# Performance work log

Measured on AMD Instinct MI355X. Metric: run time of the kernel, lower is better.

## Reference

```python
import jax, jax.numpy as jnp
import numpy as np

N_NODES = 100000
N_EDGES = 1600000
IN_CH = 128
NHIDDEN = 64
OUT_CH = 40
NLAYERS = 4
ALPHA = 0.1


def setup_inputs() -> dict:
    key = jax.random.key(0)
    ks = jax.random.split(key, 7)
    x = jax.random.normal(ks[0], (N_NODES, IN_CH), dtype=jnp.float32)
    edge_index = jax.random.randint(ks[1], (2, N_EDGES), 0, N_NODES, dtype=jnp.int64)
    batch_graph = jnp.zeros((N_NODES,), dtype=jnp.int64)
    fc1_w = jax.random.normal(ks[2], (NHIDDEN, IN_CH), dtype=jnp.float32) * (1.0 / np.sqrt(IN_CH))
    fc1_b = jax.random.normal(ks[3], (NHIDDEN,), dtype=jnp.float32) * 0.01
    conv_w = jax.random.normal(ks[4], (NLAYERS, NHIDDEN, NHIDDEN), dtype=jnp.float32) * (1.0 / np.sqrt(NHIDDEN))
    fc2_w = jax.random.normal(ks[5], (OUT_CH, NHIDDEN), dtype=jnp.float32) * (1.0 / np.sqrt(NHIDDEN))
    fc2_b = jax.random.normal(ks[6], (OUT_CH,), dtype=jnp.float32) * 0.01
    return {"x": x, "edge_index": edge_index, "batch_graph": batch_graph,
            "fc1_w": fc1_w, "fc1_b": fc1_b, "conv_w": conv_w,
            "fc2_w": fc2_w, "fc2_b": fc2_b}


def reference(x, edge_index, batch_graph, fc1_w, fc1_b, conv_w, fc2_w, fc2_b):
    # eval mode: dropout layers are identity
    n = x.shape[0]
    row, col = edge_index[0], edge_index[1]  # source, target

    # gcn_norm with add_self_loops=False: sym deg^-1/2 normalization
    deg = jax.ops.segment_sum(jnp.ones_like(row, dtype=x.dtype), col, num_segments=n)
    dinv = jnp.where(deg > 0, deg ** -0.5, 0.0)
    norm = (dinv[row] * dinv[col])[:, None]  # [E, 1]

    h = jax.nn.relu(x @ fc1_w.T + fc1_b)  # [N, nhidden]
    h0 = h
    nlayers = conv_w.shape[0]
    for i in range(nlayers):
        # GCN2Conv: aggregate, initial-residual mix, weight1 matmul (beta=1)
        agg = jax.ops.segment_sum(h[row] * norm, col, num_segments=n)
        mixed = (1.0 - ALPHA) * agg + ALPHA * h0
        h = jax.nn.relu(mixed @ conv_w[i])
    out = h @ fc2_w.T + fc2_b  # [N, out_channels]
    return out
```

## Files before the change

### kernel.cpp

```cpp
#include <hip/hip_runtime.h>
#include <hip/hip_fp16.h>

#define N_NODES 100000
#define N_EDGES 1600000
#define IN_CH   128
#define NHID    64
#define OUT_CH  40
#define NBLK    391
#define NBUCK   196
#define BCAP    8960
#define ECAP    1024


__global__ __launch_bounds__(256) void k_scan1(const int* __restrict__ cnt,
                                               int* __restrict__ rowptr,
                                               int* __restrict__ bsum) {
    __shared__ int s[256];
    int t = threadIdx.x;
    int n = blockIdx.x * 256 + t;
    int v = (n < N_NODES) ? cnt[n] : 0;
    s[t] = v;
    __syncthreads();
    for (int off = 1; off < 256; off <<= 1) {
        int add = (t >= off) ? s[t - off] : 0;
        __syncthreads();
        s[t] += add;
        __syncthreads();
    }
    int incl = s[t];
    if (n < N_NODES) rowptr[n] = incl - v;
    if (t == 255) bsum[blockIdx.x] = incl;
}

__global__ __launch_bounds__(512) void k_scan2(int* __restrict__ bsum) {
    __shared__ int s[512];
    int t = threadIdx.x;
    int v = (t < NBLK) ? bsum[t] : 0;
    s[t] = v;
    __syncthreads();
    for (int off = 1; off < 512; off <<= 1) {
        int add = (t >= off) ? s[t - off] : 0;
        __syncthreads();
        s[t] += add;
        __syncthreads();
    }
    if (t < NBLK) bsum[t] = s[t] - v;
}

__global__ __launch_bounds__(256) void k_scan3(const int* __restrict__ cnt,
                                               const int* __restrict__ bsum,
                                               int* __restrict__ rowptr,
                                               float* __restrict__ dinv) {
    int n = blockIdx.x * 256 + threadIdx.x;
    if (n < N_NODES) {
        int rp = rowptr[n] + bsum[n >> 8];
        rowptr[n] = rp;
        int c = cnt[n];
        dinv[n] = (c > 0) ? rsqrtf((float)c) : 0.0f;
    }
    if (blockIdx.x == 0 && threadIdx.x == 0) rowptr[N_NODES] = N_EDGES;
}


__global__ __launch_bounds__(256) void k_scatA(const int* __restrict__ ei,
                                               int* __restrict__ bucketCnt,
                                               int2* __restrict__ ebufA) {
    __shared__ int hist[NBUCK];
    __shared__ int base[NBUCK];
    int t = threadIdx.x;
    int chunk = blockIdx.x * 4096;
    for (int i = t; i < NBUCK; i += 256) hist[i] = 0;
    __syncthreads();
#pragma unroll 4
    for (int i = 0; i < 16; i++) {
        int e = chunk + i * 256 + t;
        if (e < N_EDGES) atomicAdd(&hist[ei[N_EDGES + e] >> 9], 1);
    }
    __syncthreads();
    for (int b = t; b < NBUCK; b += 256) {
        int h = hist[b];
        base[b] = h ? atomicAdd(&bucketCnt[b], h) : 0;
    }
    __syncthreads();
#pragma unroll 4
    for (int i = 0; i < 16; i++) {
        int e = chunk + i * 256 + t;
        if (e < N_EDGES) {
            int r = ei[e], c = ei[N_EDGES + e];
            int pos = atomicAdd(&base[c >> 9], 1);
            ebufA[(size_t)(c >> 9) * BCAP + pos] = make_int2(r, c);
        }
    }
}


__global__ __launch_bounds__(256) void k_deg(const int2* __restrict__ ebufA,
                                             const int* __restrict__ bucketCnt,
                                             int* __restrict__ cnt) {
    __shared__ int hist[512];
    int b = blockIdx.x;
    int nodeB = b * 512;
    int t = threadIdx.x;
    for (int i = t; i < 512; i += 256) hist[i] = 0;
    __syncthreads();
    int nE = bucketCnt[b];
    const int2* src = ebufA + (size_t)b * BCAP;
    for (int i = t; i < nE; i += 256) atomicAdd(&hist[src[i].y - nodeB], 1);
    __syncthreads();
    for (int i = t; i < 512; i += 256) {
        int node = nodeB + i;
        if (node < N_NODES) cnt[node] = hist[i];
    }
}


__global__ __launch_bounds__(256) void k_scatB(const int2* __restrict__ ebufA,
                                               const int* __restrict__ bucketCnt,
                                               const int* __restrict__ rowptr,
                                               int* __restrict__ e4) {
    __shared__ int lcur[512];
    int b = blockIdx.x;
    int nodeB = b * 512;
    int t = threadIdx.x;
    for (int i = t; i < 512; i += 256) {
        int node = nodeB + i;
        lcur[i] = (node < N_NODES) ? rowptr[node] : 0;
    }
    __syncthreads();
    int nE = bucketCnt[b];
    const int2* src = ebufA + (size_t)b * BCAP;
    for (int i = t; i < nE; i += 256) {
        int2 rc = src[i];
        int pos = atomicAdd(&lcur[rc.y - nodeB], 1);
        e4[pos] = rc.x;
    }
}

__device__ __forceinline__ void store_h4(__half* dst, float a, float b, float c, float d) {
    union { uint2 u; __half2 h[2]; } pk;
    pk.h[0] = __floats2half2_rn(a, b);
    pk.h[1] = __floats2half2_rn(c, d);
    *(uint2*)dst = pk.u;
}


__global__ __launch_bounds__(256, 4) void k_fc1(const float* __restrict__ x,
                                                const float* __restrict__ w,
                                                const float* __restrict__ b,
                                                const float* __restrict__ dinv,
                                                __half* __restrict__ h016,
                                                __half* __restrict__ hs1) {
    __shared__ float xs[64 * 128];
    int t = threadIdx.x;
    int nodeBase = blockIdx.x * 64;

    {
        int lane8 = t & 7, rhalf = t >> 3;
#pragma unroll
        for (int r2 = 0; r2 < 2; r2++) {
            int nl = r2 * 32 + rhalf;
            int n = nodeBase + nl;
            int swz = (nl ^ (nl >> 3)) & 7;
            float4* dstrow = (float4*)(xs + nl * 128);
            if (n < N_NODES) {
                const float4* src = (const float4*)(x + (size_t)n * IN_CH);
#pragma unroll
                for (int q = 0; q < 4; q++) dstrow[(q * 8 + lane8) ^ swz] = src[q * 8 + lane8];
            } else {
                float4 z = {0.f, 0.f, 0.f, 0.f};
#pragma unroll
                for (int q = 0; q < 4; q++) dstrow[(q * 8 + lane8) ^ swz] = z;
            }
        }
    }
    __syncthreads();

    int tx = t & 15, ty = t >> 4;
    int n0 = tx * 4, o0 = ty * 4;
    int swz0 = ((n0 + 0) ^ ((n0 + 0) >> 3)) & 7;
    int swz1 = ((n0 + 1) ^ ((n0 + 1) >> 3)) & 7;
    int swz2 = ((n0 + 2) ^ ((n0 + 2) >> 3)) & 7;
    int swz3 = ((n0 + 3) ^ ((n0 + 3) >> 3)) & 7;
    const float4* xrow0 = (const float4*)(xs + (n0 + 0) * 128);
    const float4* xrow1 = (const float4*)(xs + (n0 + 1) * 128);
    const float4* xrow2 = (const float4*)(xs + (n0 + 2) * 128);
    const float4* xrow3 = (const float4*)(xs + (n0 + 3) * 128);

    float c[4][4];
#pragma unroll
    for (int i = 0; i < 4; i++)
#pragma unroll
        for (int j = 0; j < 4; j++) c[i][j] = 0.f;

#pragma unroll 4
    for (int k = 0; k < IN_CH; k += 4) {
        int kk = k >> 2;
        float4 b0 = *(const float4*)&w[(size_t)(o0 + 0) * IN_CH + k];
        float4 b1 = *(const float4*)&w[(size_t)(o0 + 1) * IN_CH + k];
        float4 b2 = *(const float4*)&w[(size_t)(o0 + 2) * IN_CH + k];
        float4 b3 = *(const float4*)&w[(size_t)(o0 + 3) * IN_CH + k];
        float4 a0 = xrow0[kk ^ swz0];
        float4 a1 = xrow1[kk ^ swz1];
        float4 a2 = xrow2[kk ^ swz2];
        float4 a3 = xrow3[kk ^ swz3];
#pragma unroll
        for (int i = 0; i < 4; i++) {
            float4 a = (i == 0) ? a0 : (i == 1) ? a1 : (i == 2) ? a2 : a3;
            c[i][0] = fmaf(a.x, b0.x, fmaf(a.y, b0.y, fmaf(a.z, b0.z, fmaf(a.w, b0.w, c[i][0]))));
            c[i][1] = fmaf(a.x, b1.x, fmaf(a.y, b1.y, fmaf(a.z, b1.z, fmaf(a.w, b1.w, c[i][1]))));
            c[i][2] = fmaf(a.x, b2.x, fmaf(a.y, b2.y, fmaf(a.z, b2.z, fmaf(a.w, b2.w, c[i][2]))));
            c[i][3] = fmaf(a.x, b3.x, fmaf(a.y, b3.y, fmaf(a.z, b3.z, fmaf(a.w, b3.w, c[i][3]))));
        }
    }

    float4 bias = *(const float4*)&b[o0];
#pragma unroll
    for (int i = 0; i < 4; i++) {
        int n = nodeBase + n0 + i;
        if (n < N_NODES) {
            float vx = fmaxf(c[i][0] + bias.x, 0.f);
            float vy = fmaxf(c[i][1] + bias.y, 0.f);
            float vz = fmaxf(c[i][2] + bias.z, 0.f);
            float vw = fmaxf(c[i][3] + bias.w, 0.f);
            store_h4(&h016[(size_t)n * NHID + o0], vx, vy, vz, vw);
            float dn = dinv[n];
            store_h4(&hs1[(size_t)n * NHID + o0], vx * dn, vy * dn, vz * dn, vw * dn);
        }
    }
}


__global__ __launch_bounds__(256, 4) void k_conv(const __half* __restrict__ hs,
                                                 const __half* __restrict__ h0,
                                                 const int* __restrict__ rowptr,
                                                 const int* __restrict__ e4,
                                                 const float* __restrict__ W,
                                                 const float* __restrict__ dinv,
                                                 __half* __restrict__ hout,
                                                 int scaled) {
    __shared__ int   eS[ECAP];
    __shared__ float mix[32 * 68];
    int t = threadIdx.x;
    int nodeBase = blockIdx.x * 32;
    int grp = t >> 3;
    int cg = (t & 7) * 8;

    int n = nodeBase + grp;
    int s = rowptr[n], e = rowptr[n + 1];
    int base0 = rowptr[nodeBase];
    int nE = rowptr[nodeBase + 32] - base0;
    int nStage = (nE < ECAP) ? nE : ECAP;
    for (int i = t; i < nStage; i += 256) eS[i] = e4[base0 + i];

#define LOADM_G(pm, jb)                                                  \
    {                                                                    \
        _Pragma("unroll")                                                \
        for (int u = 0; u < 4; u++) {                                    \
            int idx = (jb) + u;                                          \
            pm[u] = (idx < e) ? e4[idx] : N_NODES;                       \
        }                                                                \
    }
#define LOADM(pm, jb)                                                    \
    {                                                                    \
        _Pragma("unroll")                                                \
        for (int u = 0; u < 4; u++) {                                    \
            int idx = (jb) + u;                                          \
            int m = N_NODES;                                             \
            if (idx < e) {                                               \
                int li = idx - base0;                                    \
                m = (li < ECAP) ? eS[li] : e4[idx];                      \
            }                                                            \
            pm[u] = m;                                                   \
        }                                                                \
    }
#define ISSUE(pv, pm)                                                    \
    {                                                                    \
        _Pragma("unroll")                                                \
        for (int u = 0; u < 4; u++)                                      \
            pv[u] = *(const float4*)&hs[(size_t)pm[u] * NHID + cg];      \
    }
#define ACC4(cv)                                                         \
    {                                                                    \
        _Pragma("unroll")                                                \
        for (int u = 0; u < 4; u++) {                                    \
            const __half2* hp = (const __half2*)&cv[u];                  \
            _Pragma("unroll")                                            \
            for (int q = 0; q < 4; q++) {                                \
                float2 f = __half22float2(hp[q]);                        \
                acc[q * 2 + 0] += f.x;                                   \
                acc[q * 2 + 1] += f.y;                                   \
            }                                                            \
        }                                                                \
    }

    int    pmA[4], pmB[4];
    float4 pvA[4], pvB[4];
    LOADM_G(pmA, s);     ISSUE(pvA, pmA);
    LOADM_G(pmB, s + 4); ISSUE(pvB, pmB);

    float dn = dinv[n];
    float4 h0raw = *(const float4*)&h0[(size_t)n * NHID + cg];

    float acc[8];
#pragma unroll
    for (int i = 0; i < 8; i++) acc[i] = 0.f;

    __syncthreads();

    for (int j = s; j < e; j += 8) {
        {
            float4 cv[4];
#pragma unroll
            for (int u = 0; u < 4; u++) cv[u] = pvA[u];
            int jn = j + 8;
            if (jn < e) { LOADM(pmA, jn); ISSUE(pvA, pmA); }
            ACC4(cv);
        }
        if (j + 4 < e) {
            float4 cv[4];
#pragma unroll
            for (int u = 0; u < 4; u++) cv[u] = pvB[u];
            int jn = j + 12;
            if (jn < e) { LOADM(pmB, jn); ISSUE(pvB, pmB); }
            ACC4(cv);
        }
    }
#undef LOADM_G
#undef LOADM
#undef ISSUE
#undef ACC4

    {
        const __half* h0h = (const __half*)&h0raw;
        float a = 0.9f * dn;
        float m[8];
#pragma unroll
        for (int q = 0; q < 8; q++)
            m[q] = fmaf(a, acc[q], 0.1f * __half2float(h0h[q]));
        float4 m0 = {m[0], m[1], m[2], m[3]};
        float4 m1 = {m[4], m[5], m[6], m[7]};
        *(float4*)&mix[grp * 68 + cg] = m0;
        *(float4*)&mix[grp * 68 + cg + 4] = m1;
    }
    __syncthreads();

    int tx = t & 15, ty = t >> 4;
    int o0 = tx * 4, r0 = ty * 2;
    float c[2][4];
#pragma unroll
    for (int i = 0; i < 2; i++)
#pragma unroll
        for (int j = 0; j < 4; j++) c[i][j] = 0.f;

#pragma unroll 4
    for (int k = 0; k < NHID; k += 4) {
        float4 b0 = *(const float4*)&W[(k + 0) * NHID + o0];
        float4 b1 = *(const float4*)&W[(k + 1) * NHID + o0];
        float4 b2 = *(const float4*)&W[(k + 2) * NHID + o0];
        float4 b3 = *(const float4*)&W[(k + 3) * NHID + o0];
#pragma unroll
        for (int i = 0; i < 2; i++) {
            float4 a = *(const float4*)&mix[(r0 + i) * 68 + k];
            c[i][0] = fmaf(a.x, b0.x, fmaf(a.y, b1.x, fmaf(a.z, b2.x, fmaf(a.w, b3.x, c[i][0]))));
            c[i][1] = fmaf(a.x, b0.y, fmaf(a.y, b1.y, fmaf(a.z, b2.y, fmaf(a.w, b3.y, c[i][1]))));
            c[i][2] = fmaf(a.x, b0.z, fmaf(a.y, b1.z, fmaf(a.z, b2.z, fmaf(a.w, b3.z, c[i][2]))));
            c[i][3] = fmaf(a.x, b0.w, fmaf(a.y, b1.w, fmaf(a.z, b2.w, fmaf(a.w, b3.w, c[i][3]))));
        }
    }
#pragma unroll
    for (int i = 0; i < 2; i++) {
        int n2 = nodeBase + r0 + i;
        float sc = 1.0f;
        if (scaled) sc = dinv[n2];
        store_h4(&hout[(size_t)n2 * NHID + o0],
                 fmaxf(c[i][0], 0.f) * sc, fmaxf(c[i][1], 0.f) * sc,
                 fmaxf(c[i][2], 0.f) * sc, fmaxf(c[i][3], 0.f) * sc);
    }
}


__global__ __launch_bounds__(256) void k_fc2(const __half* __restrict__ h,
                                             const float* __restrict__ w,
                                             const float* __restrict__ b,
                                             float* __restrict__ out) {
    __shared__ float wT[NHID * 44];
    __shared__ float hs[64 * 68];
    int t = threadIdx.x;
    int nodeBase = blockIdx.x * 64;

    for (int id = t; id < NHID * OUT_CH; id += 256) {
        int o = id >> 6, k = id & 63;
        wT[k * 44 + o] = w[id];
    }
    {
        int nl = t >> 2, seg = t & 3;
        int n = nodeBase + nl;
        float* dst = hs + nl * 68 + seg * 16;
        if (n < N_NODES) {
            float4 raw0 = *(const float4*)&h[(size_t)n * NHID + seg * 16];
            float4 raw1 = *(const float4*)&h[(size_t)n * NHID + seg * 16 + 8];
            const __half2* hp0 = (const __half2*)&raw0;
            const __half2* hp1 = (const __half2*)&raw1;
#pragma unroll
            for (int q = 0; q < 4; q++) {
                float2 f = __half22float2(hp0[q]);
                dst[q * 2 + 0] = f.x;
                dst[q * 2 + 1] = f.y;
            }
#pragma unroll
            for (int q = 0; q < 4; q++) {
                float2 f = __half22float2(hp1[q]);
                dst[8 + q * 2 + 0] = f.x;
                dst[8 + q * 2 + 1] = f.y;
            }
        } else {
#pragma unroll
            for (int q = 0; q < 16; q++) dst[q] = 0.f;
        }
    }
    __syncthreads();

    if (t < 160) {
        int tx = t % 10, ty = t / 10;
        int o0 = tx * 4, n0 = ty * 4;
        float c[4][4];
#pragma unroll
        for (int i = 0; i < 4; i++)
#pragma unroll
            for (int j = 0; j < 4; j++) c[i][j] = 0.f;

#pragma unroll 4
        for (int k = 0; k < NHID; k += 4) {
            float4 b0 = *(const float4*)&wT[(k + 0) * 44 + o0];
            float4 b1 = *(const float4*)&wT[(k + 1) * 44 + o0];
            float4 b2 = *(const float4*)&wT[(k + 2) * 44 + o0];
            float4 b3 = *(const float4*)&wT[(k + 3) * 44 + o0];
#pragma unroll
            for (int i = 0; i < 4; i++) {
                float4 a = *(const float4*)&hs[(n0 + i) * 68 + k];
                c[i][0] = fmaf(a.x, b0.x, fmaf(a.y, b1.x, fmaf(a.z, b2.x, fmaf(a.w, b3.x, c[i][0]))));
                c[i][1] = fmaf(a.x, b0.y, fmaf(a.y, b1.y, fmaf(a.z, b2.y, fmaf(a.w, b3.y, c[i][1]))));
                c[i][2] = fmaf(a.x, b0.z, fmaf(a.y, b1.z, fmaf(a.z, b2.z, fmaf(a.w, b3.z, c[i][2]))));
                c[i][3] = fmaf(a.x, b0.w, fmaf(a.y, b1.w, fmaf(a.z, b2.w, fmaf(a.w, b3.w, c[i][3]))));
            }
        }
        float4 bias = *(const float4*)&b[o0];
#pragma unroll
        for (int i = 0; i < 4; i++) {
            int n = nodeBase + n0 + i;
            if (n < N_NODES) {
                float4 v;
                v.x = c[i][0] + bias.x;
                v.y = c[i][1] + bias.y;
                v.z = c[i][2] + bias.z;
                v.w = c[i][3] + bias.w;
                *(float4*)&out[(size_t)n * OUT_CH + o0] = v;
            }
        }
    }
}


extern "C" void kernel_launch(void* const* d_in, const int* in_sizes, int n_in,
                              void* d_out, int out_size, void* d_ws, size_t ws_size,
                              hipStream_t stream) {
    const float* x    = (const float*)d_in[0];
    const int*   ei   = (const int*)d_in[1];
    const float* fc1w = (const float*)d_in[3];
    const float* fc1b = (const float*)d_in[4];
    const float* cw   = (const float*)d_in[5];
    const float* fc2w = (const float*)d_in[6];
    const float* fc2b = (const float*)d_in[7];
    float* out = (float*)d_out;

    char* p = (char*)d_ws;
    auto alloc = [&](size_t bytes) { char* r = p; p += (bytes + 255) & ~(size_t)255; return r; };
    __half* h016   = (__half*)alloc((size_t)N_NODES * NHID * 2);
    __half* hsA    = (__half*)alloc((size_t)(N_NODES + 1) * NHID * 2);
    __half* hsB    = (__half*)alloc((size_t)(N_NODES + 1) * NHID * 2);
    int*    e4     = (int*)   alloc((size_t)(N_EDGES + 8) * 4);
    int2*   ebufA  = (int2*)  alloc((size_t)NBUCK * BCAP * 8);
    int*    cnt    = (int*)   alloc((size_t)N_NODES * 4);
    int*    rowptr = (int*)   alloc((size_t)(N_NODES + 1) * 4);
    int*    bCnt   = (int*)   alloc((size_t)NBUCK * 4);
    float*  dinv   = (float*) alloc((size_t)N_NODES * 4);
    int*    bsum   = (int*)   alloc(512 * 4);
    __half* h4     = (__half*)ebufA;

    hipMemsetAsync(bCnt, 0, (size_t)NBUCK * 4, stream);
    hipMemsetAsync(hsA + (size_t)N_NODES * NHID, 0, NHID * 2, stream);
    hipMemsetAsync(hsB + (size_t)N_NODES * NHID, 0, NHID * 2, stream);

    k_scatA<<<(N_EDGES + 4095) / 4096, 256, 0, stream>>>(ei, bCnt, ebufA);
    k_deg  <<<NBUCK, 256, 0, stream>>>(ebufA, bCnt, cnt);
    k_scan1<<<NBLK, 256, 0, stream>>>(cnt, rowptr, bsum);
    k_scan2<<<1, 512, 0, stream>>>(bsum);
    k_scan3<<<NBLK, 256, 0, stream>>>(cnt, bsum, rowptr, dinv);
    k_scatB<<<NBUCK, 256, 0, stream>>>(ebufA, bCnt, rowptr, e4);

    int gb64 = (N_NODES + 63) / 64;
    int gb32 = N_NODES / 32;
    k_fc1 <<<gb64, 256, 0, stream>>>(x, fc1w, fc1b, dinv, h016, hsA);
    k_conv<<<gb32, 256, 0, stream>>>(hsA, h016, rowptr, e4, cw + 0 * NHID * NHID, dinv, hsB, 1);
    k_conv<<<gb32, 256, 0, stream>>>(hsB, h016, rowptr, e4, cw + 1 * NHID * NHID, dinv, hsA, 1);
    k_conv<<<gb32, 256, 0, stream>>>(hsA, h016, rowptr, e4, cw + 2 * NHID * NHID, dinv, hsB, 1);
    k_conv<<<gb32, 256, 0, stream>>>(hsB, h016, rowptr, e4, cw + 3 * NHID * NHID, dinv, h4, 0);
    k_fc2 <<<gb64, 256, 0, stream>>>(h4, fc2w, fc2b, out);
}
```

Baseline: 441.7 us.

## Compute degree with global atomics and make conv stages wavefront-local

Drops the separate degree kernel and instead counts in-degree with global atomics inside the first scatter pass. dinv is now computed in the first scan kernel, so the third scan kernel only adds the block offsets. The conv kernel gives each 64-lane wavefront its own 8-node slice with private edge staging and mix buffers, and replaces block-wide barriers with block fences. The aim is to cut a kernel launch and barrier stalls, at the cost of contended global atomics and a smaller per-wave edge cache.

```diff
diff --git a/kernel.cpp b/kernel.cpp
--- a/kernel.cpp
+++ b/kernel.cpp
@@ -9,12 +9,13 @@
 #define NBLK    391
 #define NBUCK   196
 #define BCAP    8960
-#define ECAP    1024
+#define WECAP   256
 
 
 __global__ __launch_bounds__(256) void k_scan1(const int* __restrict__ cnt,
                                                int* __restrict__ rowptr,
-                                               int* __restrict__ bsum) {
+                                               int* __restrict__ bsum,
+                                               float* __restrict__ dinv) {
     __shared__ int s[256];
     int t = threadIdx.x;
     int n = blockIdx.x * 256 + t;
@@ -28,7 +29,10 @@
         __syncthreads();
     }
     int incl = s[t];
-    if (n < N_NODES) rowptr[n] = incl - v;
+    if (n < N_NODES) {
+        rowptr[n] = incl - v;
+        dinv[n] = (v > 0) ? rsqrtf((float)v) : 0.0f;
+    }
     if (t == 255) bsum[blockIdx.x] = incl;
 }
 
@@ -47,24 +51,18 @@
     if (t < NBLK) bsum[t] = s[t] - v;
 }
 
-__global__ __launch_bounds__(256) void k_scan3(const int* __restrict__ cnt,
-                                               const int* __restrict__ bsum,
-                                               int* __restrict__ rowptr,
-                                               float* __restrict__ dinv) {
+__global__ __launch_bounds__(256) void k_scan3(const int* __restrict__ bsum,
+                                               int* __restrict__ rowptr) {
     int n = blockIdx.x * 256 + threadIdx.x;
-    if (n < N_NODES) {
-        int rp = rowptr[n] + bsum[n >> 8];
-        rowptr[n] = rp;
-        int c = cnt[n];
-        dinv[n] = (c > 0) ? rsqrtf((float)c) : 0.0f;
-    }
+    if (n < N_NODES) rowptr[n] = rowptr[n] + bsum[n >> 8];
     if (blockIdx.x == 0 && threadIdx.x == 0) rowptr[N_NODES] = N_EDGES;
 }
 
 
 __global__ __launch_bounds__(256) void k_scatA(const int* __restrict__ ei,
                                                int* __restrict__ bucketCnt,
-                                               int2* __restrict__ ebufA) {
+                                               int2* __restrict__ ebufA,
+                                               int* __restrict__ cnt) {
     __shared__ int hist[NBUCK];
     __shared__ int base[NBUCK];
     int t = threadIdx.x;
@@ -74,7 +72,11 @@
 #pragma unroll 4
     for (int i = 0; i < 16; i++) {
         int e = chunk + i * 256 + t;
-        if (e < N_EDGES) atomicAdd(&hist[ei[N_EDGES + e] >> 9], 1);
+        if (e < N_EDGES) {
+            int c = ei[N_EDGES + e];
+            atomicAdd(&hist[c >> 9], 1);
+            atomicAdd(&cnt[c], 1);
+        }
     }
     __syncthreads();
     for (int b = t; b < NBUCK; b += 256) {
@@ -90,26 +92,6 @@
             int pos = atomicAdd(&base[c >> 9], 1);
             ebufA[(size_t)(c >> 9) * BCAP + pos] = make_int2(r, c);
         }
-    }
-}
-
-
-__global__ __launch_bounds__(256) void k_deg(const int2* __restrict__ ebufA,
-                                             const int* __restrict__ bucketCnt,
-                                             int* __restrict__ cnt) {
-    __shared__ int hist[512];
-    int b = blockIdx.x;
-    int nodeB = b * 512;
-    int t = threadIdx.x;
-    for (int i = t; i < 512; i += 256) hist[i] = 0;
-    __syncthreads();
-    int nE = bucketCnt[b];
-    const int2* src = ebufA + (size_t)b * BCAP;
-    for (int i = t; i < nE; i += 256) atomicAdd(&hist[src[i].y - nodeB], 1);
-    __syncthreads();
-    for (int i = t; i < 512; i += 256) {
-        int node = nodeB + i;
-        if (node < N_NODES) cnt[node] = hist[i];
     }
 }
 
@@ -238,19 +220,22 @@
                                                  const float* __restrict__ dinv,
                                                  __half* __restrict__ hout,
                                                  int scaled) {
-    __shared__ int   eS[ECAP];
-    __shared__ float mix[32 * 68];
-    int t = threadIdx.x;
-    int nodeBase = blockIdx.x * 32;
-    int grp = t >> 3;
-    int cg = (t & 7) * 8;
-
-    int n = nodeBase + grp;
+    __shared__ int   eSw[4][WECAP];
+    __shared__ float mixs[4][8 * 68];
+    int t = threadIdx.x;
+    int wid = t >> 6, lane = t & 63;
+    int wbase = blockIdx.x * 32 + wid * 8;
+    int grp = lane >> 3;
+    int cg = (lane & 7) * 8;
+    int* eW = eSw[wid];
+    float* mix = mixs[wid];
+
+    int n = wbase + grp;
     int s = rowptr[n], e = rowptr[n + 1];
-    int base0 = rowptr[nodeBase];
-    int nE = rowptr[nodeBase + 32] - base0;
-    int nStage = (nE < ECAP) ? nE : ECAP;
-    for (int i = t; i < nStage; i += 256) eS[i] = e4[base0 + i];
+    int wb0 = rowptr[wbase];
+    int wbN = rowptr[wbase + 8] - wb0;
+    int nStage = (wbN < WECAP) ? wbN : WECAP;
+    for (int i = lane; i < nStage; i += 64) eW[i] = e4[wb0 + i];
 
 #define LOADM_G(pm, jb)                                                  \
     {                                                                    \
@@ -267,8 +252,8 @@
             int idx = (jb) + u;                                          \
             int m = N_NODES;                                             \
             if (idx < e) {                                               \
-                int li = idx - base0;                                    \
-                m = (li < ECAP) ? eS[li] : e4[idx];                      \
+                int li = idx - wb0;                                      \
+                m = (li < WECAP) ? eW[li] : e4[idx];                     \
             }                                                            \
             pm[u] = m;                                                   \
         }                                                                \
@@ -286,7 +271,7 @@
             const __half2* hp = (const __half2*)&cv[u];                  \
             _Pragma("unroll")                                            \
             for (int q = 0; q < 4; q++) {                                \
-                float2 f = __half22float2(hp[q]);                        \
+                float2 f = __half22float2(hp[q]);                       \
                 acc[q * 2 + 0] += f.x;                                   \
                 acc[q * 2 + 1] += f.y;                                   \
             }                                                            \
@@ -305,7 +290,7 @@
 #pragma unroll
     for (int i = 0; i < 8; i++) acc[i] = 0.f;
 
-    __syncthreads();
+    __threadfence_block();
 
     for (int j = s; j < e; j += 8) {
         {
@@ -342,9 +327,9 @@
         *(float4*)&mix[grp * 68 + cg] = m0;
         *(float4*)&mix[grp * 68 + cg + 4] = m1;
     }
-    __syncthreads();
-
-    int tx = t & 15, ty = t >> 4;
+    __threadfence_block();
+
+    int tx = lane & 15, ty = lane >> 4;
     int o0 = tx * 4, r0 = ty * 2;
     float c[2][4];
 #pragma unroll
@@ -369,7 +354,7 @@
     }
 #pragma unroll
     for (int i = 0; i < 2; i++) {
-        int n2 = nodeBase + r0 + i;
+        int n2 = wbase + r0 + i;
         float sc = 1.0f;
         if (scaled) sc = dinv[n2];
         store_h4(&hout[(size_t)n2 * NHID + o0],
@@ -384,7 +369,7 @@
                                              const float* __restrict__ b,
                                              float* __restrict__ out) {
     __shared__ float wT[NHID * 44];
-    __shared__ float hs[64 * 68];
+    __shared__ float hsl[64 * 68];
     int t = threadIdx.x;
     int nodeBase = blockIdx.x * 64;
 
@@ -395,7 +380,7 @@
     {
         int nl = t >> 2, seg = t & 3;
         int n = nodeBase + nl;
-        float* dst = hs + nl * 68 + seg * 16;
+        float* dst = hsl + nl * 68 + seg * 16;
         if (n < N_NODES) {
             float4 raw0 = *(const float4*)&h[(size_t)n * NHID + seg * 16];
             float4 raw1 = *(const float4*)&h[(size_t)n * NHID + seg * 16 + 8];
@@ -437,7 +422,7 @@
             float4 b3 = *(const float4*)&wT[(k + 3) * 44 + o0];
 #pragma unroll
             for (int i = 0; i < 4; i++) {
-                float4 a = *(const float4*)&hs[(n0 + i) * 68 + k];
+                float4 a = *(const float4*)&hsl[(n0 + i) * 68 + k];
                 c[i][0] = fmaf(a.x, b0.x, fmaf(a.y, b1.x, fmaf(a.z, b2.x, fmaf(a.w, b3.x, c[i][0]))));
                 c[i][1] = fmaf(a.x, b0.y, fmaf(a.y, b1.y, fmaf(a.z, b2.y, fmaf(a.w, b3.y, c[i][1]))));
                 c[i][2] = fmaf(a.x, b0.z, fmaf(a.y, b1.z, fmaf(a.z, b2.z, fmaf(a.w, b3.z, c[i][2]))));
@@ -488,14 +473,14 @@
     __half* h4     = (__half*)ebufA;
 
     hipMemsetAsync(bCnt, 0, (size_t)NBUCK * 4, stream);
+    hipMemsetAsync(cnt, 0, (size_t)N_NODES * 4, stream);
     hipMemsetAsync(hsA + (size_t)N_NODES * NHID, 0, NHID * 2, stream);
     hipMemsetAsync(hsB + (size_t)N_NODES * NHID, 0, NHID * 2, stream);
 
-    k_scatA<<<(N_EDGES + 4095) / 4096, 256, 0, stream>>>(ei, bCnt, ebufA);
-    k_deg  <<<NBUCK, 256, 0, stream>>>(ebufA, bCnt, cnt);
-    k_scan1<<<NBLK, 256, 0, stream>>>(cnt, rowptr, bsum);
+    k_scatA<<<(N_EDGES + 4095) / 4096, 256, 0, stream>>>(ei, bCnt, ebufA, cnt);
+    k_scan1<<<NBLK, 256, 0, stream>>>(cnt, rowptr, bsum, dinv);
     k_scan2<<<1, 512, 0, stream>>>(bsum);
-    k_scan3<<<NBLK, 256, 0, stream>>>(cnt, bsum, rowptr, dinv);
+    k_scan3<<<NBLK, 256, 0, stream>>>(bsum, rowptr);
     k_scatB<<<NBUCK, 256, 0, stream>>>(ebufA, bCnt, rowptr, e4);
 
     int gb64 = (N_NODES + 63) / 64;
```

Measured after the change: 466.0 us. 1.05x slower.
